# Kernel tuning notes

Hardware: AMD Instinct MI355X
Metric: run time of the kernel (lower is better)

The kernel has to match this reference:

```python
import jax, jax.numpy as jnp
import numpy as np

B, H, W, C = 2, 64, 128, 256
HEADS, K, HIDDEN = 8, 9, 1024
HD = C // HEADS
EPS = 1e-5


def _ln(z, g, b):
    m = z.mean(-1, keepdims=True)
    v = ((z - m) ** 2).mean(-1, keepdims=True)
    return (z - m) / jnp.sqrt(v + EPS) * g + b


def _bilinear(img, coords):
    # img: [hd, H, W]; coords: [H, W, K, 2] in [-1, 1] (x=width, y=height), align_corners=True
    Hh, Ww = img.shape[1], img.shape[2]
    cx = (coords[..., 0] + 1.0) * 0.5 * (Ww - 1)
    cy = (coords[..., 1] + 1.0) * 0.5 * (Hh - 1)
    x0 = jnp.floor(cx); y0 = jnp.floor(cy)
    wx = cx - x0; wy = cy - y0
    x0i = jnp.clip(x0, 0, Ww - 1).astype(jnp.int32)
    x1i = jnp.clip(x0 + 1, 0, Ww - 1).astype(jnp.int32)
    y0i = jnp.clip(y0, 0, Hh - 1).astype(jnp.int32)
    y1i = jnp.clip(y0 + 1, 0, Hh - 1).astype(jnp.int32)
    g = lambda yi, xi: img[:, yi, xi]  # [hd, H, W, K]
    return (g(y0i, x0i) * (1 - wy) * (1 - wx) + g(y0i, x1i) * (1 - wy) * wx
            + g(y1i, x0i) * wy * (1 - wx) + g(y1i, x1i) * wy * wx)


def setup_inputs() -> dict:
    key = jax.random.key(0)
    ks = jax.random.split(key, 12)
    s = 0.02
    return {
        "x": jax.random.normal(ks[0], (B, H * W, C), jnp.float32),
        "ref_point": jax.random.uniform(ks[1], (1, H, W, K, 2), jnp.float32, -1.0, 1.0),
        "ln1_g": jnp.ones((C,), jnp.float32), "ln1_b": jnp.zeros((C,), jnp.float32),
        "w_v": jax.random.normal(ks[2], (C, C), jnp.float32) * s, "b_v": jnp.zeros((C,), jnp.float32),
        "w_off": jax.random.normal(ks[3], (C, HEADS * K * 2), jnp.float32) * s, "b_off": jnp.zeros((HEADS * K * 2,), jnp.float32),
        "w_attn": jax.random.normal(ks[4], (C, HEADS * K), jnp.float32) * s, "b_attn": jnp.zeros((HEADS * K,), jnp.float32),
        "w_out": jax.random.normal(ks[5], (C, C), jnp.float32) * s, "b_out": jnp.zeros((C,), jnp.float32),
        "ln2_g": jnp.ones((C,), jnp.float32), "ln2_b": jnp.zeros((C,), jnp.float32),
        "w1": jax.random.normal(ks[6], (C, HIDDEN), jnp.float32) * s, "b1": jnp.zeros((HIDDEN,), jnp.float32),
        "w_dw": jax.random.normal(ks[7], (HIDDEN, 1, 3, 3), jnp.float32) * s, "b_dw": jnp.zeros((HIDDEN,), jnp.float32),
        "w2": jax.random.normal(ks[8], (HIDDEN, C), jnp.float32) * s, "b2": jnp.zeros((C,), jnp.float32),
    }


def reference(x, ref_point, ln1_g, ln1_b, w_v, b_v, w_off, b_off, w_attn, b_attn,
              w_out, b_out, ln2_g, ln2_b, w1, b1, w_dw, b_dw, w2, b2):
    # --- Sphere deformable self-attention branch ---
    xn = _ln(x, ln1_g, ln1_b).reshape(B, H, W, C)
    v = (xn @ w_v + b_v).reshape(B, H, W, HEADS, HD)
    v = jnp.transpose(v, (0, 3, 4, 1, 2))                               # [B, heads, hd, H, W]
    off = (xn @ w_off + b_off).reshape(B, H, W, HEADS, K, 2)
    locs = ref_point[:, :, :, None, :, :] + off                          # [B, H, W, heads, K, 2]
    locs = jnp.transpose(locs, (0, 3, 1, 2, 4, 5))                       # [B, heads, H, W, K, 2]
    attn = jax.nn.softmax((xn @ w_attn + b_attn).reshape(B, H, W, HEADS, K), axis=-1)
    sampled = jax.vmap(jax.vmap(_bilinear))(v, locs)                     # [B, heads, hd, H, W, K]
    agg = jnp.einsum('bndhwk,bhwnk->bhwnd', sampled, attn).reshape(B, H, W, C)
    x = x + ((agg @ w_out) + b_out).reshape(B, H * W, C)
    # --- LeFF branch: linear -> GELU -> circular-pad depthwise conv -> GELU -> linear ---
    y = _ln(x, ln2_g, ln2_b)
    h = jax.nn.gelu(y @ w1 + b1, approximate=False).reshape(B, H, W, HIDDEN)
    h = jnp.transpose(h, (0, 3, 1, 2))                                   # NCHW
    h = jnp.pad(h, ((0, 0), (0, 0), (0, 0), (1, 1)), mode='wrap')        # circular pad along width
    h = jnp.pad(h, ((0, 0), (0, 0), (1, 1), (0, 0)))                     # zero pad along height
    h = jax.lax.conv_general_dilated(h, w_dw, (1, 1), 'VALID',
                                     feature_group_count=HIDDEN,
                                     dimension_numbers=('NCHW', 'OIHW', 'NCHW'))
    h = jax.nn.gelu(h + b_dw[None, :, None, None], approximate=False)
    h = jnp.transpose(h, (0, 2, 3, 1)).reshape(B, H * W, HIDDEN)
    return x + h @ w2 + b2
```

## Files before the change

### kernel.cpp

```cpp
#include <hip/hip_runtime.h>
#include <hip/hip_bf16.h>
#include <hip/hip_fp8.h>
#include <type_traits>

constexpr int Bc = 2, Hc = 64, Wc = 128, Cc = 256;
constexpr int HEADS = 8, KPT = 9, HIDDEN = 1024;
constexpr int HD = Cc / HEADS;
constexpr int NPIX = Hc * Wc;
constexpr int Mrows = Bc * NPIX;
constexpr int NQKV = 512;

typedef __attribute__((ext_vector_type(4))) float f32x4;
typedef __attribute__((ext_vector_type(8))) short bf16x8;

__device__ __forceinline__ float bf2f(unsigned short u) {
    union { unsigned int i; float f; } c; c.i = ((unsigned int)u) << 16; return c.f;
}
__device__ __forceinline__ unsigned short f2bf(float f) {
    __hip_bfloat16 h = __float2bfloat16(f);
    return *reinterpret_cast<unsigned short*>(&h);
}
__device__ __forceinline__ unsigned char f2fp8(float f) {
    return __hip_fp8_e4m3(f).__x;
}
__device__ __forceinline__ float fp82f(unsigned char u) {
    __hip_fp8_e4m3 v; v.__x = u; return (float)v;
}
__device__ __forceinline__ float gelu_exact(float x) {
    return 0.5f * x * (1.0f + erff(x * 0.70710678118654752f));
}
__device__ __forceinline__ void gl2lds16(const void* g, void* l) {
    __builtin_amdgcn_global_load_lds(
        (const __attribute__((address_space(1))) unsigned int*)g,
        (__attribute__((address_space(3))) unsigned int*)l, 16, 0, 0);
}

__global__ __launch_bounds__(256) void prepln_kernel(
        const float* __restrict__ x, const float* __restrict__ ln1_g,
        const float* __restrict__ ln1_b, unsigned short* __restrict__ xn,
        const float* __restrict__ w_v, const float* __restrict__ b_v,
        const float* __restrict__ w_off, const float* __restrict__ b_off,
        const float* __restrict__ w_attn, const float* __restrict__ b_attn,
        const float* __restrict__ w_out, const float* __restrict__ w1,
        const float* __restrict__ w2, const float* __restrict__ w_dw,
        unsigned short* __restrict__ qkvT, float* __restrict__ qkvB,
        unsigned short* __restrict__ woutT, unsigned short* __restrict__ w1T,
        unsigned char* __restrict__ w2T8, float* __restrict__ wdwT) {
    const int t = threadIdx.x;
    if (blockIdx.x < Mrows / 4) {
        const int r = blockIdx.x * 4 + (t >> 6);
        const int l = t & 63;
        const size_t base = (size_t)r * Cc + l * 4;
        const float4 v = *reinterpret_cast<const float4*>(x + base);
        float s  = v.x + v.y + v.z + v.w;
        float s2 = v.x * v.x + v.y * v.y + v.z * v.z + v.w * v.w;
        #pragma unroll
        for (int o = 32; o > 0; o >>= 1) { s += __shfl_down(s, o); s2 += __shfl_down(s2, o); }
        s = __shfl(s, 0); s2 = __shfl(s2, 0);
        const float mean = s * (1.0f / Cc);
        const float rstd = rsqrtf(s2 * (1.0f / Cc) - mean * mean + 1e-5f);
        const float4 gv = *reinterpret_cast<const float4*>(ln1_g + l * 4);
        const float4 bv = *reinterpret_cast<const float4*>(ln1_b + l * 4);
        ushort4 o;
        o.x = f2bf((v.x - mean) * rstd * gv.x + bv.x);
        o.y = f2bf((v.y - mean) * rstd * gv.y + bv.y);
        o.z = f2bf((v.z - mean) * rstd * gv.z + bv.z);
        o.w = f2bf((v.w - mean) * rstd * gv.w + bv.w);
        *reinterpret_cast<ushort4*>(xn + base) = o;
        return;
    }
    const int blk = blockIdx.x - Mrows / 4;
    if (blk < NQKV) {
        const int n = blk;
        float val = 0.0f;
        if (n < 256)       val = w_v[t * 256 + n];
        else if (n < 400)  val = w_off[t * 144 + (n - 256)];
        else if (n < 472)  val = w_attn[t * 72 + (n - 400)];
        qkvT[n * 256 + t] = f2bf(val);
        if (t == 0) {
            float bv = 0.0f;
            if (n < 256)      bv = b_v[n];
            else if (n < 400) bv = b_off[n - 256];
            else if (n < 472) bv = b_attn[n - 400];
            qkvB[n] = bv;
        }
    } else if (blk < NQKV + 256) {
        const int n = blk - NQKV;
        woutT[n * 256 + t] = f2bf(w_out[t * 256 + n]);
    } else if (blk < NQKV + 256 + 1024) {
        const int n = blk - (NQKV + 256);
        w1T[n * 256 + t] = f2bf(w1[t * 1024 + n]);
    } else if (blk < NQKV + 256 + 1024 + 256) {
        const int n = blk - (NQKV + 256 + 1024);
        #pragma unroll
        for (int k = t; k < 1024; k += 256)
            w2T8[n * 1024 + k] = f2fp8(w2[k * 256 + n] * 32.0f);
    } else {
        const int j = blk - (NQKV + 256 + 1024 + 256);
        #pragma unroll
        for (int c = t; c < HIDDEN; c += 256)
            wdwT[j * HIDDEN + c] = w_dw[c * 9 + j];
    }
}

template<int BN, bool GELU, bool RESID, typename TO>
__global__ __launch_bounds__(512) void mfma_gemm(
        const unsigned short* __restrict__ A,
        const unsigned short* __restrict__ BT,
        const float* __restrict__ bias,
        const float* __restrict__ resid,
        TO* __restrict__ Out,
        int N, int K) {
    constexpr int WCOLS = (BN == 128) ? 4 : 2;
    constexpr int WROWS = 8 / WCOLS;
    constexpr int MI = 128 / (WROWS * 16);
    constexpr int NI = BN / (WCOLS * 16);
    constexpr int ACH = 2;
    constexpr int BCH = (BN / 8) / 8;
    constexpr int LA = ACH + BCH;
    constexpr int BUFB = 16384 + BN * 128;
    __shared__ __align__(16) char lds[2 * BUFB];
    const int t = threadIdx.x;
    const int w = t >> 6;
    const int l = t & 63;
    const int row0 = blockIdx.x * 128;
    const int col0 = blockIdx.y * BN;
    const int wr = (w / WCOLS) * (MI * 16);
    const int wc = (w % WCOLS) * (NI * 16);

    const int srow = l >> 3;
    const int selem = ((l & 7) ^ srow) * 8;

    auto stage = [&](char* buf, int k0) {
        unsigned short* As_ = (unsigned short*)buf;
        unsigned short* Bs_ = (unsigned short*)(buf + 16384);
        #pragma unroll
        for (int i = 0; i < ACH; ++i) {
            const int c = w + i * 8;
            const int row = c * 8 + srow;
            gl2lds16(A + (size_t)(row0 + row) * K + k0 + selem, As_ + c * 512);
        }
        #pragma unroll
        for (int i = 0; i < BCH; ++i) {
            const int c = w + i * 8;
            const int row = c * 8 + srow;
            gl2lds16(BT + (size_t)(col0 + row) * K + k0 + selem, Bs_ + c * 512);
        }
    };

    f32x4 acc[MI][NI] = {};
    const int nt = K / 64;

    stage(lds, 0);
    stage(lds + BUFB, 64);

    for (int tt = 0; tt < nt; ++tt) {
        if (tt + 1 < nt) {
            if constexpr (LA == 4) asm volatile("s_waitcnt vmcnt(4)" ::: "memory");
            else                   asm volatile("s_waitcnt vmcnt(3)" ::: "memory");
        } else {
            asm volatile("s_waitcnt vmcnt(0)" ::: "memory");
        }
        __builtin_amdgcn_s_barrier();
        __builtin_amdgcn_sched_barrier(0);

        const char* Ab = lds + (size_t)(tt & 1) * BUFB;
        const char* Bb = Ab + 16384;
        #pragma unroll
        for (int ks = 0; ks < 2; ++ks) {
            const int kb = ks * 64 + (l >> 4) * 16;
            bf16x8 af[MI], bfr[NI];
            #pragma unroll
            for (int mi = 0; mi < MI; ++mi) {
                const int row = wr + mi * 16 + (l & 15);
                af[mi] = *(const bf16x8*)(Ab + row * 128 + (kb ^ ((row & 7) << 4)));
            }
            #pragma unroll
            for (int ni = 0; ni < NI; ++ni) {
                const int row = wc + ni * 16 + (l & 15);
                bfr[ni] = *(const bf16x8*)(Bb + row * 128 + (kb ^ ((row & 7) << 4)));
            }
            #pragma unroll
            for (int mi = 0; mi < MI; ++mi)
                #pragma unroll
                for (int ni = 0; ni < NI; ++ni)
                    acc[mi][ni] = __builtin_amdgcn_mfma_f32_16x16x32_bf16(
                        af[mi], bfr[ni], acc[mi][ni], 0, 0, 0);
        }
        __builtin_amdgcn_s_barrier();
        __builtin_amdgcn_sched_barrier(0);
        if (tt + 2 < nt) stage(lds + (size_t)(tt & 1) * BUFB, (tt + 2) * 64);
    }

    constexpr int ROWB = BN * (int)sizeof(TO);
    const int lrow = (l >> 4) * 4;
    const int lcol = l & 15;
    #pragma unroll
    for (int ni = 0; ni < NI; ++ni) {
        const int col = wc + ni * 16 + lcol;
        const float bb = bias[col0 + col];
        #pragma unroll
        for (int mi = 0; mi < MI; ++mi) {
            #pragma unroll
            for (int r = 0; r < 4; ++r) {
                const int row = wr + mi * 16 + lrow + r;
                float v = acc[mi][ni][r] + bb;
                if constexpr (GELU) v = gelu_exact(v);
                if constexpr (std::is_same<TO, unsigned short>::value) {
                    *(unsigned short*)(lds + row * ROWB + ((col * 2) ^ ((row & 7) << 4))) = f2bf(v);
                } else if constexpr (std::is_same<TO, unsigned char>::value) {
                    *(unsigned char*)(lds + row * ROWB + ((col) ^ ((row & 7) << 4))) = f2fp8(v);
                } else {
                    *(float*)(lds + row * ROWB + ((col * 4) ^ ((row & 7) << 4))) = v;
                }
            }
        }
    }
    __syncthreads();
    constexpr int CPR = ROWB / 16;
    constexpr int RPI = 512 / CPR;
    const int ck = t % CPR;
    #pragma unroll
    for (int it = 0; it < 128 / RPI; ++it) {
        const int row = (t / CPR) + it * RPI;
        const int bo = ck * 16;
        const char* src = lds + row * ROWB + (bo ^ ((row & 7) << 4));
        if constexpr (std::is_same<TO, unsigned short>::value) {
            *(int4*)(Out + (size_t)(row0 + row) * N + col0 + bo / 2) = *(const int4*)src;
        } else if constexpr (std::is_same<TO, unsigned char>::value) {
            *(int4*)(Out + (size_t)(row0 + row) * N + col0 + bo) = *(const int4*)src;
        } else {
            float4 val = *(const float4*)src;
            if constexpr (RESID) {
                const float4 rv = *(const float4*)(resid + (size_t)(row0 + row) * N + col0 + bo / 4);
                val.x += rv.x; val.y += rv.y; val.z += rv.z; val.w += rv.w;
            }
            *(float4*)((float*)Out + (size_t)(row0 + row) * N + col0 + bo / 4) = val;
        }
    }
}

__global__ __launch_bounds__(512) void w2_gemm_fp8(
        const unsigned char* __restrict__ A,
        const unsigned char* __restrict__ BT,
        const float* __restrict__ bias,
        const float* __restrict__ resid,
        float* __restrict__ Out,
        int N, int K) {
    constexpr int ABYTES = 128 * 128;
    constexpr int BUFB = ABYTES + 64 * 128;
    __shared__ __align__(16) char lds[2 * BUFB];
    const int t = threadIdx.x;
    const int w = t >> 6;
    const int l = t & 63;
    const int row0 = blockIdx.x * 128;
    const int col0 = blockIdx.y * 64;
    const int wr = (w >> 1) * 32;
    const int wc = (w & 1) * 32;

    const int srow = l >> 3;
    const int sbyte = ((l & 7) ^ srow) * 16;

    auto stage = [&](char* buf, int k0) {
        unsigned char* As_ = (unsigned char*)buf;
        unsigned char* Bs_ = (unsigned char*)(buf + ABYTES);
        #pragma unroll
        for (int i = 0; i < 2; ++i) {
            const int c = w + i * 8;
            const int row = c * 8 + srow;
            gl2lds16(A + (size_t)(row0 + row) * K + k0 + sbyte, As_ + c * 1024);
        }
        {
            const int row = w * 8 + srow;
            gl2lds16(BT + (size_t)(col0 + row) * K + k0 + sbyte, Bs_ + w * 1024);
        }
    };

    f32x4 acc[2][2] = {};
    const int nt = K / 128;

    stage(lds, 0);
    stage(lds + BUFB, 128);

    for (int tt = 0; tt < nt; ++tt) {
        if (tt + 1 < nt) asm volatile("s_waitcnt vmcnt(3)" ::: "memory");
        else             asm volatile("s_waitcnt vmcnt(0)" ::: "memory");
        __builtin_amdgcn_s_barrier();
        __builtin_amdgcn_sched_barrier(0);

        const char* Ab = lds + (size_t)(tt & 1) * BUFB;
        const char* Bb = Ab + ABYTES;
        #pragma unroll
        for (int ks = 0; ks < 4; ++ks) {
            const int kb = ks * 32 + (l >> 4) * 8;
            long af[2], bfr[2];
            #pragma unroll
            for (int mi = 0; mi < 2; ++mi) {
                const int row = wr + mi * 16 + (l & 15);
                af[mi] = *(const long*)(Ab + row * 128 + (kb ^ ((row & 7) << 4)));
            }
            #pragma unroll
            for (int ni = 0; ni < 2; ++ni) {
                const int row = wc + ni * 16 + (l & 15);
                bfr[ni] = *(const long*)(Bb + row * 128 + (kb ^ ((row & 7) << 4)));
            }
            #pragma unroll
            for (int mi = 0; mi < 2; ++mi)
                #pragma unroll
                for (int ni = 0; ni < 2; ++ni)
                    acc[mi][ni] = __builtin_amdgcn_mfma_f32_16x16x32_fp8_fp8(
                        af[mi], bfr[ni], acc[mi][ni], 0, 0, 0);
        }
        __builtin_amdgcn_s_barrier();
        __builtin_amdgcn_sched_barrier(0);
        if (tt + 2 < nt) stage(lds + (size_t)(tt & 1) * BUFB, (tt + 2) * 128);
    }

    const int lrow = (l >> 4) * 4;
    const int lcol = l & 15;
    #pragma unroll
    for (int ni = 0; ni < 2; ++ni) {
        const int col = wc + ni * 16 + lcol;
        const float bb = bias[col0 + col];
        #pragma unroll
        for (int mi = 0; mi < 2; ++mi) {
            #pragma unroll
            for (int r = 0; r < 4; ++r) {
                const int row = wr + mi * 16 + lrow + r;
                *(float*)(lds + row * 256 + ((col * 4) ^ ((row & 7) << 4)))
                    = acc[mi][ni][r] * 0.03125f + bb;
            }
        }
    }
    __syncthreads();
    const int ck = t & 15;
    #pragma unroll
    for (int it = 0; it < 4; ++it) {
        const int row = (t >> 4) + it * 32;
        const int bo = ck * 16;
        float4 val = *(const float4*)(lds + row * 256 + (bo ^ ((row & 7) << 4)));
        const float4 rv = *(const float4*)(resid + (size_t)(row0 + row) * N + col0 + bo / 4);
        val.x += rv.x; val.y += rv.y; val.z += rv.z; val.w += rv.w;
        *(float4*)(Out + (size_t)(row0 + row) * N + col0 + bo / 4) = val;
    }
}

__global__ __launch_bounds__(512) void wout_ln2_kernel(
        const unsigned short* __restrict__ A,
        const unsigned short* __restrict__ BT,
        const float* __restrict__ bias,
        const float* __restrict__ resid,
        const float* __restrict__ g2, const float* __restrict__ b2,
        float* __restrict__ Out,
        unsigned short* __restrict__ Y) {
    constexpr int BM = 64, K = 256;
    constexpr int ABYTES = BM * 128;
    constexpr int BUFB = ABYTES + 256 * 128;
    __shared__ __align__(16) char lds[2 * BUFB];
    const int t = threadIdx.x;
    const int w = t >> 6;
    const int l = t & 63;
    const int row0 = blockIdx.x * BM;
    const int wr = (w >> 2) * 32;
    const int wc = (w & 3) * 64;

    const int srow = l >> 3;
    const int selem = ((l & 7) ^ srow) * 8;

    auto stage = [&](char* buf, int k0) {
        unsigned short* As_ = (unsigned short*)buf;
        unsigned short* Bs_ = (unsigned short*)(buf + ABYTES);
        {
            const int row = w * 8 + srow;
            gl2lds16(A + (size_t)(row0 + row) * K + k0 + selem, As_ + w * 512);
        }
        #pragma unroll
        for (int i = 0; i < 4; ++i) {
            const int c = w + i * 8;
            const int row = c * 8 + srow;
            gl2lds16(BT + (size_t)row * K + k0 + selem, Bs_ + c * 512);
        }
    };

    f32x4 acc[2][4] = {};
    stage(lds, 0);
    stage(lds + BUFB, 64);

    for (int tt = 0; tt < 4; ++tt) {
        if (tt + 1 < 4) asm volatile("s_waitcnt vmcnt(5)" ::: "memory");
        else            asm volatile("s_waitcnt vmcnt(0)" ::: "memory");
        __builtin_amdgcn_s_barrier();
        __builtin_amdgcn_sched_barrier(0);

        const char* Ab = lds + (size_t)(tt & 1) * BUFB;
        const char* Bb = Ab + ABYTES;
        #pragma unroll
        for (int ks = 0; ks < 2; ++ks) {
            const int kb = ks * 64 + (l >> 4) * 16;
            bf16x8 af[2], bfr[4];
            #pragma unroll
            for (int mi = 0; mi < 2; ++mi) {
                const int row = wr + mi * 16 + (l & 15);
                af[mi] = *(const bf16x8*)(Ab + row * 128 + (kb ^ ((row & 7) << 4)));
            }
            #pragma unroll
            for (int ni = 0; ni < 4; ++ni) {
                const int row = wc + ni * 16 + (l & 15);
                bfr[ni] = *(const bf16x8*)(Bb + row * 128 + (kb ^ ((row & 7) << 4)));
            }
            #pragma unroll
            for (int mi = 0; mi < 2; ++mi)
                #pragma unroll
                for (int ni = 0; ni < 4; ++ni)
                    acc[mi][ni] = __builtin_amdgcn_mfma_f32_16x16x32_bf16(
                        af[mi], bfr[ni], acc[mi][ni], 0, 0, 0);
        }
        __builtin_amdgcn_s_barrier();
        __builtin_amdgcn_sched_barrier(0);
        if (tt + 2 < 4) stage(lds + (size_t)(tt & 1) * BUFB, (tt + 2) * 64);
    }

    const int lrow = (l >> 4) * 4;
    const int lcol = l & 15;
    #pragma unroll
    for (int ni = 0; ni < 4; ++ni) {
        const int col = wc + ni * 16 + lcol;
        const float bb = bias[col];
        #pragma unroll
        for (int mi = 0; mi < 2; ++mi) {
            #pragma unroll
            for (int r = 0; r < 4; ++r) {
                const int row = wr + mi * 16 + lrow + r;
                *(float*)(lds + row * 1024 + ((col * 4) ^ ((row & 7) << 4))) = acc[mi][ni][r] + bb;
            }
        }
    }
    __syncthreads();
    const float4 gv = *reinterpret_cast<const float4*>(g2 + l * 4);
    const float4 bv = *reinterpret_cast<const float4*>(b2 + l * 4);
    #pragma unroll
    for (int it = 0; it < 8; ++it) {
        const int r = w + it * 8;
        float4 v = *(const float4*)(lds + r * 1024 + ((l * 16) ^ ((r & 7) << 4)));
        const float4 rv = *(const float4*)(resid + (size_t)(row0 + r) * Cc + l * 4);
        v.x += rv.x; v.y += rv.y; v.z += rv.z; v.w += rv.w;
        float s  = v.x + v.y + v.z + v.w;
        float s2 = v.x * v.x + v.y * v.y + v.z * v.z + v.w * v.w;
        #pragma unroll
        for (int o = 32; o > 0; o >>= 1) { s += __shfl_down(s, o); s2 += __shfl_down(s2, o); }
        s = __shfl(s, 0); s2 = __shfl(s2, 0);
        const float mean = s * (1.0f / Cc);
        const float rstd = rsqrtf(s2 * (1.0f / Cc) - mean * mean + 1e-5f);
        *(float4*)(Out + (size_t)(row0 + r) * Cc + l * 4) = v;
        ushort4 o;
        o.x = f2bf((v.x - mean) * rstd * gv.x + bv.x);
        o.y = f2bf((v.y - mean) * rstd * gv.y + bv.y);
        o.z = f2bf((v.z - mean) * rstd * gv.z + bv.z);
        o.w = f2bf((v.w - mean) * rstd * gv.w + bv.w);
        *(ushort4*)(Y + (size_t)(row0 + r) * Cc + l * 4) = o;
    }
}

__global__ __launch_bounds__(256) void sample_kernel(const unsigned short* __restrict__ F,
        const float* __restrict__ refp, unsigned short* __restrict__ agg) {
    constexpr int PPB = 4;
    constexpr int nblk = Mrows / PPB;
    const int bid = blockIdx.x;
    const int qi = (bid & 7) * (nblk / 8) + (bid >> 3);
    const int m0 = qi * PPB;
    const int b = m0 / NPIX;
    const int pix0 = m0 - b * NPIX;
    const int t = threadIdx.x;
    __shared__ int4   s_idx[PPB][72];
    __shared__ float4 s_w[PPB][72];
    __shared__ float  s_lg[PPB][72];

    for (int idx = t; idx < PPB * 72; idx += 256) {
        const int p = idx / 72, hk = idx - p * 72;
        const int head = hk / 9, k = hk - head * 9;
        const int m = m0 + p, pix = pix0 + p;
        const size_t fb = (size_t)m * NQKV;
        const unsigned int ou = *(const unsigned int*)(F + fb + 256 + head * 18 + k * 2);
        const float ox = __uint_as_float(ou << 16);
        const float oy = __uint_as_float(ou & 0xffff0000u);
        const float2 rr = *(const float2*)(refp + ((size_t)pix * KPT + k) * 2);
        const float cx = (rr.x + ox + 1.0f) * 0.5f * (Wc - 1);
        const float cy = (rr.y + oy + 1.0f) * 0.5f * (Hc - 1);
        const float fx = floorf(cx), fy = floorf(cy);
        const float wx = cx - fx, wy = cy - fy;
        const int x0 = min(max((int)fx, 0), Wc - 1);
        const int x1 = min(max((int)fx + 1, 0), Wc - 1);
        const int y0 = min(max((int)fy, 0), Hc - 1);
        const int y1 = min(max((int)fy + 1, 0), Hc - 1);
        s_idx[p][hk] = make_int4(y0 * Wc + x0, y0 * Wc + x1, y1 * Wc + x0, y1 * Wc + x1);
        s_w[p][hk] = make_float4((1.0f - wy) * (1.0f - wx), (1.0f - wy) * wx,
                                 wy * (1.0f - wx), wy * wx);
        s_lg[p][hk] = bf2f(F[fb + 400 + hk]);
    }
    __syncthreads();
    for (int idx = t; idx < PPB * 72; idx += 256) {
        const int p = idx / 72, hk = idx - p * 72;
        const int h9 = (hk / 9) * 9;
        float mx = -1e30f;
        #pragma unroll
        for (int k = 0; k < 9; ++k) mx = fmaxf(mx, s_lg[p][h9 + k]);
        float sm = 0.0f;
        #pragma unroll
        for (int k = 0; k < 9; ++k) sm += __expf(s_lg[p][h9 + k] - mx);
        const float a = __expf(s_lg[p][hk] - mx) / sm;
        float4 w = s_w[p][hk];
        w.x *= a; w.y *= a; w.z *= a; w.w *= a;
        s_w[p][hk] = w;
    }
    __syncthreads();
    const int p = t >> 6, tl = t & 63;
    const int head = tl >> 3, dq = tl & 7;
    const unsigned short* vb = F + (size_t)b * NPIX * NQKV + head * HD + dq * 4;
    float a0 = 0.f, a1 = 0.f, a2 = 0.f, a3 = 0.f;
    #pragma unroll
    for (int k = 0; k < 9; ++k) {
        const int hk = head * 9 + k;
        const int4   ix = s_idx[p][hk];
        const float4 ww = s_w[p][hk];
        {
            const uint2 u = *(const uint2*)(vb + (size_t)ix.x * NQKV);
            a0 += __uint_as_float(u.x << 16) * ww.x;
            a1 += __uint_as_float(u.x & 0xffff0000u) * ww.x;
            a2 += __uint_as_float(u.y << 16) * ww.x;
            a3 += __uint_as_float(u.y & 0xffff0000u) * ww.x;
        }
        {
            const uint2 u = *(const uint2*)(vb + (size_t)ix.y * NQKV);
            a0 += __uint_as_float(u.x << 16) * ww.y;
            a1 += __uint_as_float(u.x & 0xffff0000u) * ww.y;
            a2 += __uint_as_float(u.y << 16) * ww.y;
            a3 += __uint_as_float(u.y & 0xffff0000u) * ww.y;
        }
        {
            const uint2 u = *(const uint2*)(vb + (size_t)ix.z * NQKV);
            a0 += __uint_as_float(u.x << 16) * ww.z;
            a1 += __uint_as_float(u.x & 0xffff0000u) * ww.z;
            a2 += __uint_as_float(u.y << 16) * ww.z;
            a3 += __uint_as_float(u.y & 0xffff0000u) * ww.z;
        }
        {
            const uint2 u = *(const uint2*)(vb + (size_t)ix.w * NQKV);
            a0 += __uint_as_float(u.x << 16) * ww.w;
            a1 += __uint_as_float(u.x & 0xffff0000u) * ww.w;
            a2 += __uint_as_float(u.y << 16) * ww.w;
            a3 += __uint_as_float(u.y & 0xffff0000u) * ww.w;
        }
    }
    ushort4 o;
    o.x = f2bf(a0); o.y = f2bf(a1); o.z = f2bf(a2); o.w = f2bf(a3);
    *reinterpret_cast<ushort4*>(agg + (size_t)(m0 + p) * Cc + tl * 4) = o;
}

__global__ __launch_bounds__(256) void dwconv_kernel(const unsigned char* __restrict__ h,
        const float* __restrict__ wdwT, const float* __restrict__ bdw,
        unsigned char* __restrict__ h2) {
    constexpr int NQ = 8;
    constexpr int nblk = Mrows / NQ;
    const int bid = blockIdx.x;
    const int qi = (bid & 7) * (nblk / 8) + (bid >> 3);
    const int m0 = qi * NQ;
    const int b = m0 / NPIX;
    const int pix0 = m0 - b * NPIX;
    const int y = pix0 / Wc, x0 = pix0 - y * Wc;
    const int t = threadIdx.x;
    const int c0 = t * 4;

    float wreg[9][4];
    #pragma unroll
    for (int j = 0; j < 9; ++j) {
        const float4 wv = *reinterpret_cast<const float4*>(wdwT + j * HIDDEN + c0);
        wreg[j][0] = wv.x; wreg[j][1] = wv.y; wreg[j][2] = wv.z; wreg[j][3] = wv.w;
    }

    float acc[NQ][4] = {};
    #pragma unroll
    for (int dy = -1; dy <= 1; ++dy) {
        const int yy = y + dy;
        if (yy < 0 || yy >= Hc) continue;
        const size_t rowbase = ((size_t)b * NPIX + (size_t)yy * Wc) * HIDDEN + c0;
        #pragma unroll
        for (int j = 0; j < NQ + 2; ++j) {
            const int xx = (x0 + j - 1 + Wc) & (Wc - 1);
            const uchar4 hv = *reinterpret_cast<const uchar4*>(h + rowbase + (size_t)xx * HIDDEN);
            const float f0 = fp82f(hv.x), f1 = fp82f(hv.y), f2 = fp82f(hv.z), f3 = fp82f(hv.w);
            #pragma unroll
            for (int q = 0; q < NQ; ++q) {
                if (q >= j - 2 && q <= j) {
                    const int wj = (dy + 1) * 3 + (j - q);
                    acc[q][0] += f0 * wreg[wj][0];
                    acc[q][1] += f1 * wreg[wj][1];
                    acc[q][2] += f2 * wreg[wj][2];
                    acc[q][3] += f3 * wreg[wj][3];
                }
            }
        }
    }
    const float4 bb = *reinterpret_cast<const float4*>(bdw + c0);
    #pragma unroll
    for (int q = 0; q < NQ; ++q) {
        uchar4 o;
        o.x = f2fp8(gelu_exact(acc[q][0] + bb.x));
        o.y = f2fp8(gelu_exact(acc[q][1] + bb.y));
        o.z = f2fp8(gelu_exact(acc[q][2] + bb.z));
        o.w = f2fp8(gelu_exact(acc[q][3] + bb.w));
        *reinterpret_cast<uchar4*>(h2 + (size_t)(m0 + q) * HIDDEN + c0) = o;
    }
}

extern "C" void kernel_launch(void* const* d_in, const int* in_sizes, int n_in,
                              void* d_out, int out_size, void* d_ws, size_t ws_size,
                              hipStream_t stream) {
    const float* x      = (const float*)d_in[0];
    const float* refp   = (const float*)d_in[1];
    const float* ln1_g  = (const float*)d_in[2];
    const float* ln1_b  = (const float*)d_in[3];
    const float* w_v    = (const float*)d_in[4];
    const float* b_v    = (const float*)d_in[5];
    const float* w_off  = (const float*)d_in[6];
    const float* b_off  = (const float*)d_in[7];
    const float* w_attn = (const float*)d_in[8];
    const float* b_attn = (const float*)d_in[9];
    const float* w_out  = (const float*)d_in[10];
    const float* b_out  = (const float*)d_in[11];
    const float* ln2_g  = (const float*)d_in[12];
    const float* ln2_b  = (const float*)d_in[13];
    const float* w1     = (const float*)d_in[14];
    const float* b1     = (const float*)d_in[15];
    const float* w_dw   = (const float*)d_in[16];
    const float* b_dw   = (const float*)d_in[17];
    const float* w2     = (const float*)d_in[18];
    const float* b2     = (const float*)d_in[19];
    float* out = (float*)d_out;

    char* wsb = (char*)d_ws;
    unsigned short* Abuf = (unsigned short*)(wsb);
    unsigned short* F    = (unsigned short*)(wsb + (8ull  << 20));
    unsigned short* ybuf = (unsigned short*)(wsb + (8ull  << 20));
    unsigned char*  hbuf = (unsigned char*)(wsb + (32ull << 20));
    unsigned char*  h2   = (unsigned char*)(wsb + (16ull << 20));
    size_t woff = 64ull << 20;
    unsigned short* qkvT = (unsigned short*)(wsb + woff); woff += (size_t)NQKV * 256 * 2;
    unsigned short* woutT= (unsigned short*)(wsb + woff); woff += 256 * 256 * 2;
    unsigned short* w1T  = (unsigned short*)(wsb + woff); woff += 1024 * 256 * 2;
    unsigned char*  w2T8 = (unsigned char*)(wsb + woff);  woff += 256 * 1024;
    float*          wdwT = (float*)(wsb + woff);          woff += 9 * 1024 * 4;
    float*          qkvB = (float*)(wsb + woff);

    prepln_kernel<<<Mrows / 4 + NQKV + 256 + 1024 + 256 + 9, 256, 0, stream>>>(
        x, ln1_g, ln1_b, Abuf,
        w_v, b_v, w_off, b_off, w_attn, b_attn, w_out, w1, w2, w_dw,
        qkvT, qkvB, woutT, w1T, w2T8, wdwT);
    mfma_gemm<128, false, false, unsigned short><<<dim3(Mrows / 128, NQKV / 128), 512, 0, stream>>>(
        Abuf, qkvT, qkvB, nullptr, F, NQKV, 256);
    sample_kernel<<<Mrows / 4, 256, 0, stream>>>(F, refp, Abuf);
    wout_ln2_kernel<<<Mrows / 64, 512, 0, stream>>>(
        Abuf, woutT, b_out, x, ln2_g, ln2_b, out, ybuf);
    mfma_gemm<128, true, false, unsigned char><<<dim3(Mrows / 128, 1024 / 128), 512, 0, stream>>>(
        ybuf, w1T, b1, nullptr, hbuf, 1024, 256);
    dwconv_kernel<<<Mrows / 8, 256, 0, stream>>>(hbuf, wdwT, b_dw, h2);
    w2_gemm_fp8<<<dim3(Mrows / 128, 256 / 64), 512, 0, stream>>>(
        h2, w2T8, b2, out, out, 256, 1024);
}
```

Measured before the change: 117.5 us.

## Split QKV output into FP8 value plane and BF16 offset/attn plane; halve wout tile

A dedicated QKV GEMM now writes the value projection as FP8 into a compact 256-wide buffer and the offset/attention logits as BF16 into a separate 256-wide buffer. The sampling kernel's random gathers then read 4 bytes per lane instead of 8, cutting gather bandwidth and cache footprint. Separately, the wout+LN2 kernel's row tile is reduced from 64 to 32 to launch more blocks. FP8 storage of values adds quantization error in the sampled features, and the smaller tile reloads the weight matrix more often.

```diff
diff --git a/kernel.cpp b/kernel.cpp
--- a/kernel.cpp
+++ b/kernel.cpp
@@ -240,6 +240,136 @@
     }
 }
 
+__global__ __launch_bounds__(512) void qkv_gemm(
+        const unsigned short* __restrict__ A,
+        const unsigned short* __restrict__ BT,
+        const float* __restrict__ bias,
+        unsigned char* __restrict__ Fv,
+        unsigned short* __restrict__ Foa,
+        int K) {
+    constexpr int BN = 128;
+    constexpr int MI = 4, NI = 2;
+    constexpr int BUFB = 16384 + BN * 128;
+    __shared__ __align__(16) char lds[2 * BUFB];
+    const int t = threadIdx.x;
+    const int w = t >> 6;
+    const int l = t & 63;
+    const int row0 = blockIdx.x * 128;
+    const int col0 = blockIdx.y * BN;
+    const int wr = (w / 4) * 64;
+    const int wc = (w % 4) * 32;
+
+    const int srow = l >> 3;
+    const int selem = ((l & 7) ^ srow) * 8;
+
+    auto stage = [&](char* buf, int k0) {
+        unsigned short* As_ = (unsigned short*)buf;
+        unsigned short* Bs_ = (unsigned short*)(buf + 16384);
+        #pragma unroll
+        for (int i = 0; i < 2; ++i) {
+            const int c = w + i * 8;
+            const int row = c * 8 + srow;
+            gl2lds16(A + (size_t)(row0 + row) * K + k0 + selem, As_ + c * 512);
+        }
+        #pragma unroll
+        for (int i = 0; i < 2; ++i) {
+            const int c = w + i * 8;
+            const int row = c * 8 + srow;
+            gl2lds16(BT + (size_t)(col0 + row) * K + k0 + selem, Bs_ + c * 512);
+        }
+    };
+
+    f32x4 acc[MI][NI] = {};
+    stage(lds, 0);
+    stage(lds + BUFB, 64);
+
+    for (int tt = 0; tt < 4; ++tt) {
+        if (tt + 1 < 4) asm volatile("s_waitcnt vmcnt(4)" ::: "memory");
+        else            asm volatile("s_waitcnt vmcnt(0)" ::: "memory");
+        __builtin_amdgcn_s_barrier();
+        __builtin_amdgcn_sched_barrier(0);
+
+        const char* Ab = lds + (size_t)(tt & 1) * BUFB;
+        const char* Bb = Ab + 16384;
+        #pragma unroll
+        for (int ks = 0; ks < 2; ++ks) {
+            const int kb = ks * 64 + (l >> 4) * 16;
+            bf16x8 af[MI], bfr[NI];
+            #pragma unroll
+            for (int mi = 0; mi < MI; ++mi) {
+                const int row = wr + mi * 16 + (l & 15);
+                af[mi] = *(const bf16x8*)(Ab + row * 128 + (kb ^ ((row & 7) << 4)));
+            }
+            #pragma unroll
+            for (int ni = 0; ni < NI; ++ni) {
+                const int row = wc + ni * 16 + (l & 15);
+                bfr[ni] = *(const bf16x8*)(Bb + row * 128 + (kb ^ ((row & 7) << 4)));
+            }
+            #pragma unroll
+            for (int mi = 0; mi < MI; ++mi)
+                #pragma unroll
+                for (int ni = 0; ni < NI; ++ni)
+                    acc[mi][ni] = __builtin_amdgcn_mfma_f32_16x16x32_bf16(
+                        af[mi], bfr[ni], acc[mi][ni], 0, 0, 0);
+        }
+        __builtin_amdgcn_s_barrier();
+        __builtin_amdgcn_sched_barrier(0);
+        if (tt + 2 < 4) stage(lds + (size_t)(tt & 1) * BUFB, (tt + 2) * 64);
+    }
+
+    const int lrow = (l >> 4) * 4;
+    const int lcol = l & 15;
+    if (col0 < 256) {
+        #pragma unroll
+        for (int ni = 0; ni < NI; ++ni) {
+            const int col = wc + ni * 16 + lcol;
+            const float bb = bias[col0 + col];
+            #pragma unroll
+            for (int mi = 0; mi < MI; ++mi) {
+                #pragma unroll
+                for (int r = 0; r < 4; ++r) {
+                    const int row = wr + mi * 16 + lrow + r;
+                    *(unsigned char*)(lds + row * 128 + (col ^ ((row & 7) << 4)))
+                        = f2fp8(acc[mi][ni][r] + bb);
+                }
+            }
+        }
+        __syncthreads();
+        const int ck = t & 7;
+        #pragma unroll
+        for (int it = 0; it < 2; ++it) {
+            const int row = (t >> 3) + it * 64;
+            const int bo = ck * 16;
+            *(int4*)(Fv + (size_t)(row0 + row) * 256 + col0 + bo)
+                = *(const int4*)(lds + row * 128 + (bo ^ ((row & 7) << 4)));
+        }
+    } else {
+        #pragma unroll
+        for (int ni = 0; ni < NI; ++ni) {
+            const int col = wc + ni * 16 + lcol;
+            const float bb = bias[col0 + col];
+            #pragma unroll
+            for (int mi = 0; mi < MI; ++mi) {
+                #pragma unroll
+                for (int r = 0; r < 4; ++r) {
+                    const int row = wr + mi * 16 + lrow + r;
+                    *(unsigned short*)(lds + row * 256 + ((col * 2) ^ ((row & 7) << 4)))
+                        = f2bf(acc[mi][ni][r] + bb);
+                }
+            }
+        }
+        __syncthreads();
+        const int ck = t & 15;
+        #pragma unroll
+        for (int it = 0; it < 4; ++it) {
+            const int row = (t >> 4) + it * 32;
+            const int bo = ck * 16;
+            *(int4*)(Foa + (size_t)(row0 + row) * 256 + (col0 - 256) + bo / 2)
+                = *(const int4*)(lds + row * 256 + (bo ^ ((row & 7) << 4)));
+        }
+    }
+}
+
 __global__ __launch_bounds__(512) void w2_gemm_fp8(
         const unsigned char* __restrict__ A,
         const unsigned char* __restrict__ BT,
@@ -353,7 +483,7 @@
         const float* __restrict__ g2, const float* __restrict__ b2,
         float* __restrict__ Out,
         unsigned short* __restrict__ Y) {
-    constexpr int BM = 64, K = 256;
+    constexpr int BM = 32, K = 256;
     constexpr int ABYTES = BM * 128;
     constexpr int BUFB = ABYTES + 256 * 128;
     __shared__ __align__(16) char lds[2 * BUFB];
@@ -361,7 +491,7 @@
     const int w = t >> 6;
     const int l = t & 63;
     const int row0 = blockIdx.x * BM;
-    const int wr = (w >> 2) * 32;
+    const int wr = (w >> 2) * 16;
     const int wc = (w & 3) * 64;
 
     const int srow = l >> 3;
@@ -370,7 +500,7 @@
     auto stage = [&](char* buf, int k0) {
         unsigned short* As_ = (unsigned short*)buf;
         unsigned short* Bs_ = (unsigned short*)(buf + ABYTES);
-        {
+        if (w < 4) {
             const int row = w * 8 + srow;
             gl2lds16(A + (size_t)(row0 + row) * K + k0 + selem, As_ + w * 512);
         }
@@ -382,13 +512,17 @@
         }
     };
 
-    f32x4 acc[2][4] = {};
+    f32x4 acc[1][4] = {};
     stage(lds, 0);
     stage(lds + BUFB, 64);
 
     for (int tt = 0; tt < 4; ++tt) {
-        if (tt + 1 < 4) asm volatile("s_waitcnt vmcnt(5)" ::: "memory");
-        else            asm volatile("s_waitcnt vmcnt(0)" ::: "memory");
+        if (tt + 1 < 4) {
+            if (w < 4) asm volatile("s_waitcnt vmcnt(5)" ::: "memory");
+            else       asm volatile("s_waitcnt vmcnt(4)" ::: "memory");
+        } else {
+            asm volatile("s_waitcnt vmcnt(0)" ::: "memory");
+        }
         __builtin_amdgcn_s_barrier();
         __builtin_amdgcn_sched_barrier(0);
 
@@ -397,11 +531,10 @@
         #pragma unroll
         for (int ks = 0; ks < 2; ++ks) {
             const int kb = ks * 64 + (l >> 4) * 16;
-            bf16x8 af[2], bfr[4];
-            #pragma unroll
-            for (int mi = 0; mi < 2; ++mi) {
-                const int row = wr + mi * 16 + (l & 15);
-                af[mi] = *(const bf16x8*)(Ab + row * 128 + (kb ^ ((row & 7) << 4)));
+            bf16x8 af, bfr[4];
+            {
+                const int row = wr + (l & 15);
+                af = *(const bf16x8*)(Ab + row * 128 + (kb ^ ((row & 7) << 4)));
             }
             #pragma unroll
             for (int ni = 0; ni < 4; ++ni) {
@@ -409,11 +542,9 @@
                 bfr[ni] = *(const bf16x8*)(Bb + row * 128 + (kb ^ ((row & 7) << 4)));
             }
             #pragma unroll
-            for (int mi = 0; mi < 2; ++mi)
-                #pragma unroll
-                for (int ni = 0; ni < 4; ++ni)
-                    acc[mi][ni] = __builtin_amdgcn_mfma_f32_16x16x32_bf16(
-                        af[mi], bfr[ni], acc[mi][ni], 0, 0, 0);
+            for (int ni = 0; ni < 4; ++ni)
+                acc[0][ni] = __builtin_amdgcn_mfma_f32_16x16x32_bf16(
+                    af, bfr[ni], acc[0][ni], 0, 0, 0);
         }
         __builtin_amdgcn_s_barrier();
         __builtin_amdgcn_sched_barrier(0);
@@ -427,19 +558,16 @@
         const int col = wc + ni * 16 + lcol;
         const float bb = bias[col];
         #pragma unroll
-        for (int mi = 0; mi < 2; ++mi) {
-            #pragma unroll
-            for (int r = 0; r < 4; ++r) {
-                const int row = wr + mi * 16 + lrow + r;
-                *(float*)(lds + row * 1024 + ((col * 4) ^ ((row & 7) << 4))) = acc[mi][ni][r] + bb;
-            }
+        for (int r = 0; r < 4; ++r) {
+            const int row = wr + lrow + r;
+            *(float*)(lds + row * 1024 + ((col * 4) ^ ((row & 7) << 4))) = acc[0][ni][r] + bb;
         }
     }
     __syncthreads();
     const float4 gv = *reinterpret_cast<const float4*>(g2 + l * 4);
     const float4 bv = *reinterpret_cast<const float4*>(b2 + l * 4);
     #pragma unroll
-    for (int it = 0; it < 8; ++it) {
+    for (int it = 0; it < 4; ++it) {
         const int r = w + it * 8;
         float4 v = *(const float4*)(lds + r * 1024 + ((l * 16) ^ ((r & 7) << 4)));
         const float4 rv = *(const float4*)(resid + (size_t)(row0 + r) * Cc + l * 4);
@@ -461,7 +589,8 @@
     }
 }
 
-__global__ __launch_bounds__(256) void sample_kernel(const unsigned short* __restrict__ F,
+__global__ __launch_bounds__(256) void sample_kernel(const unsigned char* __restrict__ Fv,
+        const unsigned short* __restrict__ Foa,
         const float* __restrict__ refp, unsigned short* __restrict__ agg) {
     constexpr int PPB = 4;
     constexpr int nblk = Mrows / PPB;
@@ -479,8 +608,8 @@
         const int p = idx / 72, hk = idx - p * 72;
         const int head = hk / 9, k = hk - head * 9;
         const int m = m0 + p, pix = pix0 + p;
-        const size_t fb = (size_t)m * NQKV;
-        const unsigned int ou = *(const unsigned int*)(F + fb + 256 + head * 18 + k * 2);
+        const size_t fb = (size_t)m * 256;
+        const unsigned int ou = *(const unsigned int*)(Foa + fb + head * 18 + k * 2);
         const float ox = __uint_as_float(ou << 16);
         const float oy = __uint_as_float(ou & 0xffff0000u);
         const float2 rr = *(const float2*)(refp + ((size_t)pix * KPT + k) * 2);
@@ -495,7 +624,7 @@
         s_idx[p][hk] = make_int4(y0 * Wc + x0, y0 * Wc + x1, y1 * Wc + x0, y1 * Wc + x1);
         s_w[p][hk] = make_float4((1.0f - wy) * (1.0f - wx), (1.0f - wy) * wx,
                                  wy * (1.0f - wx), wy * wx);
-        s_lg[p][hk] = bf2f(F[fb + 400 + hk]);
+        s_lg[p][hk] = bf2f(Foa[fb + 144 + hk]);
     }
     __syncthreads();
     for (int idx = t; idx < PPB * 72; idx += 256) {
@@ -515,7 +644,7 @@
     __syncthreads();
     const int p = t >> 6, tl = t & 63;
     const int head = tl >> 3, dq = tl & 7;
-    const unsigned short* vb = F + (size_t)b * NPIX * NQKV + head * HD + dq * 4;
+    const unsigned char* vb = Fv + (size_t)b * NPIX * 256 + head * HD + dq * 4;
     float a0 = 0.f, a1 = 0.f, a2 = 0.f, a3 = 0.f;
     #pragma unroll
     for (int k = 0; k < 9; ++k) {
@@ -523,32 +652,24 @@
         const int4   ix = s_idx[p][hk];
         const float4 ww = s_w[p][hk];
         {
-            const uint2 u = *(const uint2*)(vb + (size_t)ix.x * NQKV);
-            a0 += __uint_as_float(u.x << 16) * ww.x;
-            a1 += __uint_as_float(u.x & 0xffff0000u) * ww.x;
-            a2 += __uint_as_float(u.y << 16) * ww.x;
-            a3 += __uint_as_float(u.y & 0xffff0000u) * ww.x;
+            const uchar4 u = *(const uchar4*)(vb + (size_t)ix.x * 256);
+            a0 += fp82f(u.x) * ww.x; a1 += fp82f(u.y) * ww.x;
+            a2 += fp82f(u.z) * ww.x; a3 += fp82f(u.w) * ww.x;
         }
         {
-            const uint2 u = *(const uint2*)(vb + (size_t)ix.y * NQKV);
-            a0 += __uint_as_float(u.x << 16) * ww.y;
-            a1 += __uint_as_float(u.x & 0xffff0000u) * ww.y;
-            a2 += __uint_as_float(u.y << 16) * ww.y;
-            a3 += __uint_as_float(u.y & 0xffff0000u) * ww.y;
+            const uchar4 u = *(const uchar4*)(vb + (size_t)ix.y * 256);
+            a0 += fp82f(u.x) * ww.y; a1 += fp82f(u.y) * ww.y;
+            a2 += fp82f(u.z) * ww.y; a3 += fp82f(u.w) * ww.y;
         }
         {
-            const uint2 u = *(const uint2*)(vb + (size_t)ix.z * NQKV);
-            a0 += __uint_as_float(u.x << 16) * ww.z;
-            a1 += __uint_as_float(u.x & 0xffff0000u) * ww.z;
-            a2 += __uint_as_float(u.y << 16) * ww.z;
-            a3 += __uint_as_float(u.y & 0xffff0000u) * ww.z;
+            const uchar4 u = *(const uchar4*)(vb + (size_t)ix.z * 256);
+            a0 += fp82f(u.x) * ww.z; a1 += fp82f(u.y) * ww.z;
+            a2 += fp82f(u.z) * ww.z; a3 += fp82f(u.w) * ww.z;
         }
         {
-            const uint2 u = *(const uint2*)(vb + (size_t)ix.w * NQKV);
-            a0 += __uint_as_float(u.x << 16) * ww.w;
-            a1 += __uint_as_float(u.x & 0xffff0000u) * ww.w;
-            a2 += __uint_as_float(u.y << 16) * ww.w;
-            a3 += __uint_as_float(u.y & 0xffff0000u) * ww.w;
+            const uchar4 u = *(const uchar4*)(vb + (size_t)ix.w * 256);
+            a0 += fp82f(u.x) * ww.w; a1 += fp82f(u.y) * ww.w;
+            a2 += fp82f(u.z) * ww.w; a3 += fp82f(u.w) * ww.w;
         }
     }
     ushort4 o;
@@ -639,7 +760,8 @@
 
     char* wsb = (char*)d_ws;
     unsigned short* Abuf = (unsigned short*)(wsb);
-    unsigned short* F    = (unsigned short*)(wsb + (8ull  << 20));
+    unsigned short* Foa  = (unsigned short*)(wsb + (8ull  << 20));
+    unsigned char*  Fv   = (unsigned char*)(wsb + (16ull << 20));
     unsigned short* ybuf = (unsigned short*)(wsb + (8ull  << 20));
     unsigned char*  hbuf = (unsigned char*)(wsb + (32ull << 20));
     unsigned char*  h2   = (unsigned char*)(wsb + (16ull << 20));
@@ -655,10 +777,10 @@
         x, ln1_g, ln1_b, Abuf,
         w_v, b_v, w_off, b_off, w_attn, b_attn, w_out, w1, w2, w_dw,
         qkvT, qkvB, woutT, w1T, w2T8, wdwT);
-    mfma_gemm<128, false, false, unsigned short><<<dim3(Mrows / 128, NQKV / 128), 512, 0, stream>>>(
-        Abuf, qkvT, qkvB, nullptr, F, NQKV, 256);
-    sample_kernel<<<Mrows / 4, 256, 0, stream>>>(F, refp, Abuf);
-    wout_ln2_kernel<<<Mrows / 64, 512, 0, stream>>>(
+    qkv_gemm<<<dim3(Mrows / 128, NQKV / 128), 512, 0, stream>>>(
+        Abuf, qkvT, qkvB, Fv, Foa, 256);
+    sample_kernel<<<Mrows / 4, 256, 0, stream>>>(Fv, Foa, refp, Abuf);
+    wout_ln2_kernel<<<Mrows / 32, 512, 0, stream>>>(
         Abuf, woutT, b_out, x, ln2_g, ln2_b, out, ybuf);
     mfma_gemm<128, true, false, unsigned char><<<dim3(Mrows / 128, 1024 / 128), 512, 0, stream>>>(
         ybuf, w1T, b1, nullptr, hbuf, 1024, 256);
```

New measurement: 113.3 us. 3.6% less time.
